# Kernel optimization log

Hardware: AMD Instinct MI355X
Metric: run time of the kernel (lower is better)

Reference implementation:

```python
import jax, jax.numpy as jnp
import numpy as np

N = 50000   # nodes
E = 600000  # edges
D = 128     # in = hidden = out channels
L = 3       # num_layers
LN_EPS = 1e-5


def setup_inputs() -> dict:
    key = jax.random.key(0)
    ks = jax.random.split(key, 4)
    x = jax.random.normal(ks[0], (N, D), dtype=jnp.float32)
    edge_index = jax.random.randint(ks[1], (2, E), 0, N, dtype=jnp.int32)
    # GCNConv linear weights (glorot-ish scale) and biases, one per layer
    Ws = jax.random.normal(ks[2], (L, D, D), dtype=jnp.float32) / np.sqrt(D)
    bs = jnp.zeros((L, D), dtype=jnp.float32)
    # LayerNorm affine params per layer
    ln_w = jnp.ones((L, D), dtype=jnp.float32)
    ln_b = jnp.zeros((L, D), dtype=jnp.float32)
    # PReLU (single shared slope per layer, torch default init 0.25)
    alphas = jnp.full((L,), 0.25, dtype=jnp.float32)
    return {"x": x, "edge_index": edge_index, "Ws": Ws, "bs": bs,
            "ln_w": ln_w, "ln_b": ln_b, "alphas": alphas}


def reference(x, edge_index, Ws, bs, ln_w, ln_b, alphas):
    # --- gcn_norm: add self-loops, symmetric D^{-1/2} (A+I) D^{-1/2} ---
    loop = jnp.arange(N, dtype=edge_index.dtype)
    src = jnp.concatenate([edge_index[0], loop])  # [E+N]
    dst = jnp.concatenate([edge_index[1], loop])  # [E+N]
    deg = jax.ops.segment_sum(jnp.ones_like(dst, dtype=x.dtype), dst,
                              num_segments=N)
    dinv = jnp.where(deg > 0, jax.lax.rsqrt(jnp.maximum(deg, 1.0)), 0.0)
    norm = (dinv[src] * dinv[dst])[:, None]  # [E+N, 1]

    h = x
    for l in range(L):
        # GCNConv: linear -> gather -> scale -> scatter-add -> bias
        h = h @ Ws[l]                                   # [N, D]
        msg = h[src] * norm                             # [E+N, D]
        h = jax.ops.segment_sum(msg, dst, num_segments=N) + bs[l]
        # LayerNorm over feature dim
        mu = jnp.mean(h, axis=-1, keepdims=True)
        var = jnp.mean((h - mu) ** 2, axis=-1, keepdims=True)
        h = (h - mu) * jax.lax.rsqrt(var + LN_EPS) * ln_w[l] + ln_b[l]
        # PReLU
        h = jnp.where(h >= 0, h, alphas[l] * h)
    return h
```

## Files before the change

### kernel.cpp

```cpp
#include <hip/hip_runtime.h>
#include <hip/hip_bf16.h>

#define NN 50000
#define EE 600000
#define DD 128
#define LL 3
#define LN_EPS 1e-5f
#define CAP 64
#define CNTS 16
#define ALD 136
#define POOL 16
#define NTILES (NN / POOL)
#define FILLB ((EE + 255) / 256)

typedef __attribute__((ext_vector_type(8))) short short8;
typedef __attribute__((ext_vector_type(4))) float floatx4;
typedef __attribute__((ext_vector_type(4))) unsigned uintx4;

__device__ inline unsigned short f2bf(float f) {
    union { float f; unsigned u; } a; a.f = f;
    unsigned r = a.u + 0x7fffu + ((a.u >> 16) & 1u);
    return (unsigned short)(r >> 16);
}

__device__ inline uintx4 make_srsrc(const void* p, unsigned bytes) {
    unsigned long long a = (unsigned long long)p;
    uintx4 r;
    r.x = (unsigned)a;
    r.y = (unsigned)(a >> 32);
    r.z = bytes;
    r.w = 0x00020000u;
    return r;
}

__device__ inline uintx4 bload(uintx4 srsrc, unsigned voff) {
    uintx4 r;
    asm volatile("buffer_load_dwordx4 %0, %1, %2, 0 offen"
                 : "=v"(r) : "v"(voff), "s"(srsrc));
    return r;
}

#define WAITV(n) do { \
    asm volatile("s_waitcnt vmcnt(" #n ")" ::: "memory"); \
    __builtin_amdgcn_sched_barrier(0); \
} while (0)


__global__ __launch_bounds__(256) void init_kernel(const float* __restrict__ W,
                                                   unsigned short* __restrict__ Wt,
                                                   int* __restrict__ cnt,
                                                   unsigned short* __restrict__ tbufA,
                                                   unsigned short* __restrict__ tbufB) {
    int tid = blockIdx.x * 256 + threadIdx.x;
    for (int i = tid; i < NN * CNTS / 4; i += gridDim.x * 256)
        ((int4*)cnt)[i] = make_int4(0, 0, 0, 0);
    for (int i = tid; i < 16 * DD / 2; i += gridDim.x * 256) {
        ((int*)&tbufA[(size_t)NN * DD])[i] = 0;
        ((int*)&tbufB[(size_t)NN * DD])[i] = 0;
    }
    for (int i = tid; i < LL * DD * DD; i += gridDim.x * 256) {
        int l = i >> 14, n = (i >> 7) & 127, k = i & 127;
        Wt[i] = f2bf(W[(l << 14) + k * DD + n]);
    }
}


__global__ __launch_bounds__(256) void fill_kernel(
    const int* __restrict__ src, const int* __restrict__ dst,
    int* __restrict__ cnt, int* __restrict__ csrc) {
    int e = blockIdx.x * 256 + threadIdx.x;
    if (e < EE) {
        int d = dst[e];
        int s = src[e];
        int pos = atomicAdd(&cnt[d * CNTS], 1);
        csrc[(size_t)d * CAP + pos] = s;
    }
}


__global__ __launch_bounds__(256) void gemm0_kernel(
    const float* __restrict__ A, const unsigned short* __restrict__ Wt,
    const int* __restrict__ cnt, unsigned short* __restrict__ Cb) {
    __shared__ unsigned short alds[POOL * ALD];
    __shared__ float s_dinv[POOL];
    int tid = threadIdx.x;
    int lane = tid & 63;
    int w = tid >> 6;
    int nodebase = blockIdx.x * POOL;

    if (tid < POOL)
        s_dinv[tid] = rsqrtf((float)(cnt[(nodebase + tid) * CNTS] + 1));

    {
        int row = tid >> 4;
        int kc = (tid & 15) * 8;
        const float* ap = &A[(size_t)(nodebase + row) * DD + kc];
        float4 v0 = *(const float4*)&ap[0];
        float4 v1 = *(const float4*)&ap[4];
        float fv[8] = {v0.x, v0.y, v0.z, v0.w, v1.x, v1.y, v1.z, v1.w};
        unsigned short uv[8];
        #pragma unroll
        for (int q = 0; q < 8; q++) uv[q] = f2bf(fv[q]);
        *(uint4*)&alds[row * ALD + kc] = *(uint4*)&uv[0];
    }
    __syncthreads();

    int cbase = w * 32;
    int kq = (lane >> 4) * 8;
    int mrow = lane & 15;
    floatx4 acc[2] = {{0.f,0.f,0.f,0.f},{0.f,0.f,0.f,0.f}};
    #pragma unroll
    for (int t = 0; t < 4; t++) {
        short8 a = *(const short8*)&alds[mrow * ALD + t * 32 + kq];
        #pragma unroll
        for (int j = 0; j < 2; j++) {
            short8 b = *(const short8*)&Wt[(cbase + j * 16 + (lane & 15)) * DD + t * 32 + kq];
            acc[j] = __builtin_amdgcn_mfma_f32_16x16x32_bf16(a, b, acc[j], 0, 0, 0);
        }
    }
    __syncthreads();

    {
        int r0 = (lane >> 4) * 4;
        #pragma unroll
        for (int i = 0; i < 4; i++) {
            float dvr = s_dinv[r0 + i];
            #pragma unroll
            for (int j = 0; j < 2; j++)
                alds[(r0 + i) * ALD + cbase + j * 16 + (lane & 15)] = f2bf(acc[j][i] * dvr);
        }
    }
    __syncthreads();
    {
        int srow = tid >> 4;
        int scol = (tid & 15) * 8;
        *(uint4*)&Cb[(size_t)(nodebase + srow) * DD + scol] =
            *(uint4*)&alds[srow * ALD + scol];
    }
}


__device__ inline void acc_row(float* acc, uintx4 t) {
    #pragma unroll
    for (int q = 0; q < 4; q++) {
        union { unsigned x; float f; } lo, hi;
        lo.x = t[q] << 16;
        hi.x = t[q] & 0xffff0000u;
        acc[2 * q]     += lo.f;
        acc[2 * q + 1] += hi.f;
    }
}

__device__ inline void agg_node(uintx4 srsrc,
                                const int* __restrict__ cnt, const int* __restrict__ csrc,
                                const float* bv, const float* wv, const float* cv,
                                float alpha, int node, int f8, float* yv, float* dv_out) {
    int deg = cnt[node * CNTS];
    float dv = rsqrtf((float)(deg + 1));
    *dv_out = dv;
    const int* row = &csrc[(size_t)node * CAP];
    unsigned vbase = (unsigned)f8 * 2u;

    int4 i0 = *(const int4*)&row[0];
    int4 i1 = *(const int4*)&row[4];
    int4 i2 = *(const int4*)&row[8];
    int4 i3 = *(const int4*)&row[12];
    int idx[16] = {i0.x, i0.y, i0.z, i0.w, i1.x, i1.y, i1.z, i1.w,
                   i2.x, i2.y, i2.z, i2.w, i3.x, i3.y, i3.z, i3.w};
    unsigned voff[16];
    #pragma unroll
    for (int k = 0; k < 16; k++) {
        int s = (k < deg) ? idx[k] : NN;
        voff[k] = ((unsigned)s << 8) + vbase;
    }
    unsigned voffself = ((unsigned)node << 8) + vbase;

    WAITV(0);
    uintx4 ts = bload(srsrc, voffself);
    uintx4 t0 = bload(srsrc, voff[0]),  t1 = bload(srsrc, voff[1]);
    uintx4 t2 = bload(srsrc, voff[2]),  t3 = bload(srsrc, voff[3]);
    uintx4 t4 = bload(srsrc, voff[4]),  t5 = bload(srsrc, voff[5]);
    uintx4 t6 = bload(srsrc, voff[6]),  t7 = bload(srsrc, voff[7]);

    float acc[8] = {};
    WAITV(8);
    acc_row(acc, ts);
    WAITV(4);
    acc_row(acc, t0); acc_row(acc, t1); acc_row(acc, t2); acc_row(acc, t3);
    uintx4 u0 = bload(srsrc, voff[8]),  u1 = bload(srsrc, voff[9]);
    uintx4 u2 = bload(srsrc, voff[10]), u3 = bload(srsrc, voff[11]);
    WAITV(4);
    acc_row(acc, t4); acc_row(acc, t5); acc_row(acc, t6); acc_row(acc, t7);
    uintx4 w0 = bload(srsrc, voff[12]), w1 = bload(srsrc, voff[13]);
    uintx4 w2 = bload(srsrc, voff[14]), w3 = bload(srsrc, voff[15]);
    WAITV(4);
    acc_row(acc, u0); acc_row(acc, u1); acc_row(acc, u2); acc_row(acc, u3);
    WAITV(0);
    acc_row(acc, w0); acc_row(acc, w1); acc_row(acc, w2); acc_row(acc, w3);

    for (int k = 16; k < deg; k += 4) {
        int4 ss = *(const int4*)&row[k];
        unsigned v0 = ((unsigned)ss.x << 8) + vbase;
        unsigned v1 = ((unsigned)((k + 1 < deg) ? ss.y : NN) << 8) + vbase;
        unsigned v2 = ((unsigned)((k + 2 < deg) ? ss.z : NN) << 8) + vbase;
        unsigned v3 = ((unsigned)((k + 3 < deg) ? ss.w : NN) << 8) + vbase;
        uintx4 a0 = bload(srsrc, v0), a1 = bload(srsrc, v1);
        uintx4 a2 = bload(srsrc, v2), a3 = bload(srsrc, v3);
        WAITV(0);
        acc_row(acc, a0); acc_row(acc, a1); acc_row(acc, a2); acc_row(acc, a3);
    }

    float a[8];
    float s1 = 0.f, s2 = 0.f;
    #pragma unroll
    for (int q = 0; q < 8; q++) {
        a[q] = fmaf(acc[q], dv, bv[q]);
        s1 += a[q]; s2 += a[q] * a[q];
    }
    #pragma unroll
    for (int off = 8; off > 0; off >>= 1) {
        s1 += __shfl_xor(s1, off, 16);
        s2 += __shfl_xor(s2, off, 16);
    }
    float mu = s1 * (1.f / DD);
    float var = s2 * (1.f / DD) - mu * mu;
    float rstd = rsqrtf(var + LN_EPS);
    #pragma unroll
    for (int q = 0; q < 8; q++) {
        float y = (a[q] - mu) * rstd * wv[q] + cv[q];
        yv[q] = (y >= 0.f) ? y : alpha * y;
    }
}


__global__ __launch_bounds__(256) void aggemm_kernel(
    const unsigned short* __restrict__ Tb, const int* __restrict__ cnt,
    const int* __restrict__ csrc,
    const float* __restrict__ bias, const float* __restrict__ lnw,
    const float* __restrict__ lnb, const float* __restrict__ alphas, int layer,
    const unsigned short* __restrict__ Wt, unsigned short* __restrict__ Tout) {
    __shared__ unsigned short alds[POOL * ALD];
    __shared__ float s_dinv[POOL];
    int tid = threadIdx.x;
    int g = tid >> 4;
    int lane16 = tid & 15;
    int f8 = lane16 * 8;
    int nodebase = blockIdx.x * POOL;

    uintx4 srsrc = make_srsrc(Tb, (NN + 1) * DD * 2);

    float4 b0 = *(const float4*)&bias[f8];
    float4 b1 = *(const float4*)&bias[f8 + 4];
    float4 w0 = *(const float4*)&lnw[f8];
    float4 w1 = *(const float4*)&lnw[f8 + 4];
    float4 c0 = *(const float4*)&lnb[f8];
    float4 c1 = *(const float4*)&lnb[f8 + 4];
    float bv[8] = {b0.x, b0.y, b0.z, b0.w, b1.x, b1.y, b1.z, b1.w};
    float wv[8] = {w0.x, w0.y, w0.z, w0.w, w1.x, w1.y, w1.z, w1.w};
    float cv[8] = {c0.x, c0.y, c0.z, c0.w, c1.x, c1.y, c1.z, c1.w};
    float alpha = alphas[layer];

    {
        int node = nodebase + g;
        float yv[8], dv;
        agg_node(srsrc, cnt, csrc, bv, wv, cv, alpha, node, f8, yv, &dv);
        if (lane16 == 0) s_dinv[g] = dv;
        unsigned short pv[8];
        #pragma unroll
        for (int q = 0; q < 8; q++) pv[q] = f2bf(yv[q]);
        *(uint4*)&alds[g * ALD + f8] = *(uint4*)&pv[0];
    }
    __syncthreads();

    int lane = tid & 63;
    int w = tid >> 6;
    int cbase = w * 32;
    int kq = (lane >> 4) * 8;
    int mrow = lane & 15;
    floatx4 acc[2] = {{0.f,0.f,0.f,0.f},{0.f,0.f,0.f,0.f}};
    #pragma unroll
    for (int t = 0; t < 4; t++) {
        short8 a = *(const short8*)&alds[mrow * ALD + t * 32 + kq];
        #pragma unroll
        for (int j = 0; j < 2; j++) {
            short8 b = *(const short8*)&Wt[(cbase + j * 16 + (lane & 15)) * DD + t * 32 + kq];
            acc[j] = __builtin_amdgcn_mfma_f32_16x16x32_bf16(a, b, acc[j], 0, 0, 0);
        }
    }
    __syncthreads();

    {
        int r0 = (lane >> 4) * 4;
        #pragma unroll
        for (int i = 0; i < 4; i++) {
            float dvr = s_dinv[r0 + i];
            #pragma unroll
            for (int j = 0; j < 2; j++)
                alds[(r0 + i) * ALD + cbase + j * 16 + (lane & 15)] = f2bf(acc[j][i] * dvr);
        }
    }
    __syncthreads();
    {
        int srow = tid >> 4;
        int scol = (tid & 15) * 8;
        *(uint4*)&Tout[(size_t)(nodebase + srow) * DD + scol] =
            *(uint4*)&alds[srow * ALD + scol];
    }
}


__global__ __launch_bounds__(256) void agg_final_kernel(
    const unsigned short* __restrict__ Tb, const int* __restrict__ cnt,
    const int* __restrict__ csrc,
    const float* __restrict__ bias, const float* __restrict__ lnw,
    const float* __restrict__ lnb, const float* __restrict__ alphas, int layer,
    float* __restrict__ out) {
    int g = threadIdx.x >> 4;
    int lane16 = threadIdx.x & 15;
    int f8 = lane16 * 8;
    int node = blockIdx.x * POOL + g;

    uintx4 srsrc = make_srsrc(Tb, (NN + 1) * DD * 2);

    float4 b0 = *(const float4*)&bias[f8];
    float4 b1 = *(const float4*)&bias[f8 + 4];
    float4 w0 = *(const float4*)&lnw[f8];
    float4 w1 = *(const float4*)&lnw[f8 + 4];
    float4 c0 = *(const float4*)&lnb[f8];
    float4 c1 = *(const float4*)&lnb[f8 + 4];
    float bv[8] = {b0.x, b0.y, b0.z, b0.w, b1.x, b1.y, b1.z, b1.w};
    float wv[8] = {w0.x, w0.y, w0.z, w0.w, w1.x, w1.y, w1.z, w1.w};
    float cv[8] = {c0.x, c0.y, c0.z, c0.w, c1.x, c1.y, c1.z, c1.w};

    float yv[8], dv;
    agg_node(srsrc, cnt, csrc, bv, wv, cv, alphas[layer], node, f8, yv, &dv);

    float* op = &out[(size_t)node * DD + f8];
    *(float4*)&op[0] = make_float4(yv[0], yv[1], yv[2], yv[3]);
    *(float4*)&op[4] = make_float4(yv[4], yv[5], yv[6], yv[7]);
}


extern "C" void kernel_launch(void* const* d_in, const int* in_sizes, int n_in,
                              void* d_out, int out_size, void* d_ws, size_t ws_size,
                              hipStream_t stream) {
    const float* x    = (const float*)d_in[0];
    const int*   ei   = (const int*)d_in[1];
    const float* Ws   = (const float*)d_in[2];
    const float* bs   = (const float*)d_in[3];
    const float* lnw  = (const float*)d_in[4];
    const float* lnb  = (const float*)d_in[5];
    const float* alphas = (const float*)d_in[6];
    float* out = (float*)d_out;

    const int* src = ei;
    const int* dst = ei + EE;

    char* ws = (char*)d_ws;
    size_t off = 0;
    auto alloc = [&](size_t bytes) -> void* {
        void* p = ws + off;
        off = (off + bytes + 255) & ~(size_t)255;
        return p;
    };
    int* cnt  = (int*)alloc((size_t)NN * CNTS * sizeof(int));
    int* csrc = (int*)alloc((size_t)NN * CAP * sizeof(int));
    unsigned short* wt    = (unsigned short*)alloc((size_t)LL * DD * DD * sizeof(unsigned short));
    unsigned short* tbufA = (unsigned short*)alloc((size_t)(NN + 16) * DD * sizeof(unsigned short));
    unsigned short* tbufB = (unsigned short*)alloc((size_t)(NN + 16) * DD * sizeof(unsigned short));

    init_kernel<<<512, 256, 0, stream>>>(Ws, wt, cnt, tbufA, tbufB);
    fill_kernel<<<FILLB, 256, 0, stream>>>(src, dst, cnt, csrc);
    gemm0_kernel<<<NTILES, 256, 0, stream>>>(x, wt, cnt, tbufA);

    aggemm_kernel<<<NTILES, 256, 0, stream>>>(tbufA, cnt, csrc,
                                              bs + 0 * DD, lnw + 0 * DD, lnb + 0 * DD,
                                              alphas, 0, wt + 1 * DD * DD, tbufB);
    aggemm_kernel<<<NTILES, 256, 0, stream>>>(tbufB, cnt, csrc,
                                              bs + 1 * DD, lnw + 1 * DD, lnb + 1 * DD,
                                              alphas, 1, wt + 2 * DD * DD, tbufA);
    agg_final_kernel<<<NTILES, 256, 0, stream>>>(tbufA, cnt, csrc,
                                                 bs + 2 * DD, lnw + 2 * DD, lnb + 2 * DD,
                                                 alphas, 2, out);
}
```

Measured before the change: 230.0 us.

## Aggregate four nodes per wave with one dword per lane per neighbor

Changes the gather mapping from 16 lanes per node with dwordx4 loads to a full 64-lane wave per node, where each lane loads one dword (two bf16 features). Each wave handles four nodes and issues 68 outstanding loads before staged waits. Neighbor indices are broadcast with readlane, and LayerNorm reduces across the full wave. Degrees above 16 fall back to a slow serial scalar loop. The change is meant to raise memory-level parallelism and coalescing, at the cost of many more load instructions and higher register pressure.

After: 241.3 us. +4.9%, slower.

```diff
diff --git a/kernel.cpp b/kernel.cpp
--- a/kernel.cpp
+++ b/kernel.cpp
@@ -33,17 +33,25 @@
     return r;
 }
 
-__device__ inline uintx4 bload(uintx4 srsrc, unsigned voff) {
-    uintx4 r;
-    asm volatile("buffer_load_dwordx4 %0, %1, %2, 0 offen"
+__device__ inline unsigned bload1(uintx4 srsrc, unsigned voff) {
+    unsigned r;
+    asm volatile("buffer_load_dword %0, %1, %2, 0 offen"
                  : "=v"(r) : "v"(voff), "s"(srsrc));
     return r;
 }
 
-#define WAITV(n) do { \
+#define WAITVM(n) do { \
     asm volatile("s_waitcnt vmcnt(" #n ")" ::: "memory"); \
     __builtin_amdgcn_sched_barrier(0); \
 } while (0)
+
+__device__ inline void upadd(unsigned v, float& x, float& y) {
+    union { unsigned u; float f; } lo, hi;
+    lo.u = v << 16;
+    hi.u = v & 0xffff0000u;
+    x += lo.f;
+    y += hi.f;
+}
 
 
 __global__ __launch_bounds__(256) void init_kernel(const float* __restrict__ W,
@@ -140,96 +148,88 @@
 }
 
 
-__device__ inline void acc_row(float* acc, uintx4 t) {
-    #pragma unroll
-    for (int q = 0; q < 4; q++) {
-        union { unsigned x; float f; } lo, hi;
-        lo.x = t[q] << 16;
-        hi.x = t[q] & 0xffff0000u;
-        acc[2 * q]     += lo.f;
-        acc[2 * q + 1] += hi.f;
-    }
-}
-
-__device__ inline void agg_node(uintx4 srsrc,
-                                const int* __restrict__ cnt, const int* __restrict__ csrc,
-                                const float* bv, const float* wv, const float* cv,
-                                float alpha, int node, int f8, float* yv, float* dv_out) {
-    int deg = cnt[node * CNTS];
-    float dv = rsqrtf((float)(deg + 1));
-    *dv_out = dv;
-    const int* row = &csrc[(size_t)node * CAP];
-    unsigned vbase = (unsigned)f8 * 2u;
-
-    int4 i0 = *(const int4*)&row[0];
-    int4 i1 = *(const int4*)&row[4];
-    int4 i2 = *(const int4*)&row[8];
-    int4 i3 = *(const int4*)&row[12];
-    int idx[16] = {i0.x, i0.y, i0.z, i0.w, i1.x, i1.y, i1.z, i1.w,
-                   i2.x, i2.y, i2.z, i2.w, i3.x, i3.y, i3.z, i3.w};
-    unsigned voff[16];
-    #pragma unroll
-    for (int k = 0; k < 16; k++) {
-        int s = (k < deg) ? idx[k] : NN;
-        voff[k] = ((unsigned)s << 8) + vbase;
-    }
-    unsigned voffself = ((unsigned)node << 8) + vbase;
-
-    WAITV(0);
-    uintx4 ts = bload(srsrc, voffself);
-    uintx4 t0 = bload(srsrc, voff[0]),  t1 = bload(srsrc, voff[1]);
-    uintx4 t2 = bload(srsrc, voff[2]),  t3 = bload(srsrc, voff[3]);
-    uintx4 t4 = bload(srsrc, voff[4]),  t5 = bload(srsrc, voff[5]);
-    uintx4 t6 = bload(srsrc, voff[6]),  t7 = bload(srsrc, voff[7]);
-
-    float acc[8] = {};
-    WAITV(8);
-    acc_row(acc, ts);
-    WAITV(4);
-    acc_row(acc, t0); acc_row(acc, t1); acc_row(acc, t2); acc_row(acc, t3);
-    uintx4 u0 = bload(srsrc, voff[8]),  u1 = bload(srsrc, voff[9]);
-    uintx4 u2 = bload(srsrc, voff[10]), u3 = bload(srsrc, voff[11]);
-    WAITV(4);
-    acc_row(acc, t4); acc_row(acc, t5); acc_row(acc, t6); acc_row(acc, t7);
-    uintx4 w0 = bload(srsrc, voff[12]), w1 = bload(srsrc, voff[13]);
-    uintx4 w2 = bload(srsrc, voff[14]), w3 = bload(srsrc, voff[15]);
-    WAITV(4);
-    acc_row(acc, u0); acc_row(acc, u1); acc_row(acc, u2); acc_row(acc, u3);
-    WAITV(0);
-    acc_row(acc, w0); acc_row(acc, w1); acc_row(acc, w2); acc_row(acc, w3);
-
-    for (int k = 16; k < deg; k += 4) {
-        int4 ss = *(const int4*)&row[k];
-        unsigned v0 = ((unsigned)ss.x << 8) + vbase;
-        unsigned v1 = ((unsigned)((k + 1 < deg) ? ss.y : NN) << 8) + vbase;
-        unsigned v2 = ((unsigned)((k + 2 < deg) ? ss.z : NN) << 8) + vbase;
-        unsigned v3 = ((unsigned)((k + 3 < deg) ? ss.w : NN) << 8) + vbase;
-        uintx4 a0 = bload(srsrc, v0), a1 = bload(srsrc, v1);
-        uintx4 a2 = bload(srsrc, v2), a3 = bload(srsrc, v3);
-        WAITV(0);
-        acc_row(acc, a0); acc_row(acc, a1); acc_row(acc, a2); acc_row(acc, a3);
-    }
-
-    float a[8];
-    float s1 = 0.f, s2 = 0.f;
-    #pragma unroll
-    for (int q = 0; q < 8; q++) {
-        a[q] = fmaf(acc[q], dv, bv[q]);
-        s1 += a[q]; s2 += a[q] * a[q];
-    }
-    #pragma unroll
-    for (int off = 8; off > 0; off >>= 1) {
-        s1 += __shfl_xor(s1, off, 16);
-        s2 += __shfl_xor(s2, off, 16);
+__device__ inline void agg_wave4(uintx4 srsrc, const unsigned short* __restrict__ Tb,
+                                 const int* __restrict__ cnt, const int* __restrict__ csrc,
+                                 int n0, int lane,
+                                 float* A0, float* A1, float* DV) {
+    unsigned l4 = (unsigned)lane << 2;
+    int lane16 = lane & 15;
+
+    int deg[4], iv[4];
+    #pragma unroll
+    for (int j = 0; j < 4; j++)
+        deg[j] = cnt[(size_t)(n0 + j) * CNTS];
+    #pragma unroll
+    for (int j = 0; j < 4; j++) {
+        int raw = csrc[(size_t)(n0 + j) * CAP + lane16];
+        iv[j] = (lane16 < deg[j]) ? raw : NN;
+        DV[j] = rsqrtf((float)(deg[j] + 1));
+    }
+    WAITVM(0);
+
+    unsigned r[4][17];
+    #pragma unroll
+    for (int j = 0; j < 4; j++) {
+        r[j][0] = bload1(srsrc, ((unsigned)(n0 + j) << 8) + l4);
+        #pragma unroll
+        for (int q = 0; q < 16; q++) {
+            int s = __builtin_amdgcn_readlane(iv[j], q);
+            r[j][q + 1] = bload1(srsrc, ((unsigned)s << 8) + l4);
+        }
+    }
+
+    float b0[4], b1[4];
+    WAITVM(51);
+    b0[0] = 0.f; b1[0] = 0.f;
+    #pragma unroll
+    for (int q = 0; q < 17; q++) upadd(r[0][q], b0[0], b1[0]);
+    WAITVM(34);
+    b0[1] = 0.f; b1[1] = 0.f;
+    #pragma unroll
+    for (int q = 0; q < 17; q++) upadd(r[1][q], b0[1], b1[1]);
+    WAITVM(17);
+    b0[2] = 0.f; b1[2] = 0.f;
+    #pragma unroll
+    for (int q = 0; q < 17; q++) upadd(r[2][q], b0[2], b1[2]);
+    WAITVM(0);
+    b0[3] = 0.f; b1[3] = 0.f;
+    #pragma unroll
+    for (int q = 0; q < 17; q++) upadd(r[3][q], b0[3], b1[3]);
+
+    #pragma unroll
+    for (int j = 0; j < 4; j++) {
+        if (deg[j] > 16) {
+            for (int k = 16; k < deg[j]; k++) {
+                int s = csrc[(size_t)(n0 + j) * CAP + k];
+                unsigned v = *(const unsigned*)((const char*)Tb + ((size_t)s << 8) + l4);
+                upadd(v, b0[j], b1[j]);
+            }
+        }
+    }
+    #pragma unroll
+    for (int j = 0; j < 4; j++) { A0[j] = b0[j]; A1[j] = b1[j]; }
+}
+
+__device__ inline void ln_prelu(float acc0, float acc1, float dv,
+                                float bv0, float bv1, float wv0, float wv1,
+                                float cv0, float cv1, float alpha,
+                                float& y0, float& y1) {
+    float a0 = fmaf(acc0, dv, bv0);
+    float a1 = fmaf(acc1, dv, bv1);
+    float s1 = a0 + a1;
+    float s2 = a0 * a0 + a1 * a1;
+    #pragma unroll
+    for (int off = 32; off > 0; off >>= 1) {
+        s1 += __shfl_xor(s1, off, 64);
+        s2 += __shfl_xor(s2, off, 64);
     }
     float mu = s1 * (1.f / DD);
     float var = s2 * (1.f / DD) - mu * mu;
     float rstd = rsqrtf(var + LN_EPS);
-    #pragma unroll
-    for (int q = 0; q < 8; q++) {
-        float y = (a[q] - mu) * rstd * wv[q] + cv[q];
-        yv[q] = (y >= 0.f) ? y : alpha * y;
-    }
+    y0 = (a0 - mu) * rstd * wv0 + cv0;
+    y1 = (a1 - mu) * rstd * wv1 + cv1;
+    y0 = (y0 >= 0.f) ? y0 : alpha * y0;
+    y1 = (y1 >= 0.f) ? y1 : alpha * y1;
 }
 
 
@@ -242,38 +242,34 @@
     __shared__ unsigned short alds[POOL * ALD];
     __shared__ float s_dinv[POOL];
     int tid = threadIdx.x;
-    int g = tid >> 4;
-    int lane16 = tid & 15;
-    int f8 = lane16 * 8;
-    int nodebase = blockIdx.x * POOL;
-
-    uintx4 srsrc = make_srsrc(Tb, (NN + 1) * DD * 2);
-
-    float4 b0 = *(const float4*)&bias[f8];
-    float4 b1 = *(const float4*)&bias[f8 + 4];
-    float4 w0 = *(const float4*)&lnw[f8];
-    float4 w1 = *(const float4*)&lnw[f8 + 4];
-    float4 c0 = *(const float4*)&lnb[f8];
-    float4 c1 = *(const float4*)&lnb[f8 + 4];
-    float bv[8] = {b0.x, b0.y, b0.z, b0.w, b1.x, b1.y, b1.z, b1.w};
-    float wv[8] = {w0.x, w0.y, w0.z, w0.w, w1.x, w1.y, w1.z, w1.w};
-    float cv[8] = {c0.x, c0.y, c0.z, c0.w, c1.x, c1.y, c1.z, c1.w};
-    float alpha = alphas[layer];
-
-    {
-        int node = nodebase + g;
-        float yv[8], dv;
-        agg_node(srsrc, cnt, csrc, bv, wv, cv, alpha, node, f8, yv, &dv);
-        if (lane16 == 0) s_dinv[g] = dv;
-        unsigned short pv[8];
-        #pragma unroll
-        for (int q = 0; q < 8; q++) pv[q] = f2bf(yv[q]);
-        *(uint4*)&alds[g * ALD + f8] = *(uint4*)&pv[0];
-    }
-    __syncthreads();
-
     int lane = tid & 63;
     int w = tid >> 6;
+    int nodebase = blockIdx.x * POOL;
+    int f2 = lane * 2;
+
+    uintx4 srsrc = make_srsrc(Tb, (NN + 1) * DD * 2);
+
+    float2 bp = *(const float2*)&bias[f2];
+    float2 wp = *(const float2*)&lnw[f2];
+    float2 cp = *(const float2*)&lnb[f2];
+    float alpha = alphas[layer];
+
+    {
+        int n0 = nodebase + (w << 2);
+        float A0[4], A1[4], DV[4];
+        agg_wave4(srsrc, Tb, cnt, csrc, n0, lane, A0, A1, DV);
+        #pragma unroll
+        for (int j = 0; j < 4; j++) {
+            float y0, y1;
+            ln_prelu(A0[j], A1[j], DV[j], bp.x, bp.y, wp.x, wp.y, cp.x, cp.y,
+                     alpha, y0, y1);
+            unsigned packed = (unsigned)f2bf(y0) | ((unsigned)f2bf(y1) << 16);
+            *(unsigned*)&alds[((w << 2) + j) * ALD + f2] = packed;
+            if (lane == 0) s_dinv[(w << 2) + j] = DV[j];
+        }
+    }
+    __syncthreads();
+
     int cbase = w * 32;
     int kq = (lane >> 4) * 8;
     int mrow = lane & 15;
@@ -315,29 +311,29 @@
     const float* __restrict__ bias, const float* __restrict__ lnw,
     const float* __restrict__ lnb, const float* __restrict__ alphas, int layer,
     float* __restrict__ out) {
-    int g = threadIdx.x >> 4;
-    int lane16 = threadIdx.x & 15;
-    int f8 = lane16 * 8;
-    int node = blockIdx.x * POOL + g;
+    int tid = threadIdx.x;
+    int lane = tid & 63;
+    int w = tid >> 6;
+    int f2 = lane * 2;
+    int n0 = blockIdx.x * POOL + (w << 2);
 
     uintx4 srsrc = make_srsrc(Tb, (NN + 1) * DD * 2);
 
-    float4 b0 = *(const float4*)&bias[f8];
-    float4 b1 = *(const float4*)&bias[f8 + 4];
-    float4 w0 = *(const float4*)&lnw[f8];
-    float4 w1 = *(const float4*)&lnw[f8 + 4];
-    float4 c0 = *(const float4*)&lnb[f8];
-    float4 c1 = *(const float4*)&lnb[f8 + 4];
-    float bv[8] = {b0.x, b0.y, b0.z, b0.w, b1.x, b1.y, b1.z, b1.w};
-    float wv[8] = {w0.x, w0.y, w0.z, w0.w, w1.x, w1.y, w1.z, w1.w};
-    float cv[8] = {c0.x, c0.y, c0.z, c0.w, c1.x, c1.y, c1.z, c1.w};
-
-    float yv[8], dv;
-    agg_node(srsrc, cnt, csrc, bv, wv, cv, alphas[layer], node, f8, yv, &dv);
-
-    float* op = &out[(size_t)node * DD + f8];
-    *(float4*)&op[0] = make_float4(yv[0], yv[1], yv[2], yv[3]);
-    *(float4*)&op[4] = make_float4(yv[4], yv[5], yv[6], yv[7]);
+    float2 bp = *(const float2*)&bias[f2];
+    float2 wp = *(const float2*)&lnw[f2];
+    float2 cp = *(const float2*)&lnb[f2];
+    float alpha = alphas[layer];
+
+    float A0[4], A1[4], DV[4];
+    agg_wave4(srsrc, Tb, cnt, csrc, n0, lane, A0, A1, DV);
+
+    #pragma unroll
+    for (int j = 0; j < 4; j++) {
+        float y0, y1;
+        ln_prelu(A0[j], A1[j], DV[j], bp.x, bp.y, wp.x, wp.y, cp.x, cp.y,
+                 alpha, y0, y1);
+        *(float2*)&out[(size_t)(n0 + j) * DD + f2] = make_float2(y0, y1);
+    }
 }
 
 
```

## Retile first-layer GEMM to 80 rows per block with 5 waves

Applied to the files above, without the earlier changes.

The first-layer GEMM now processes 80 node rows per block using 320 threads, where each wave owns 16 rows and computes all 128 output columns, instead of 16 rows per block with each wave covering 32 columns. This cuts the block count by a factor of five and amortizes the per-block setup and weight reads across more rows. Each wave now reads the full weight matrix and holds 8 accumulators, which raises register use and per-wave weight traffic.

Measured after the change: 235.3 us. 1.02x slower.

```diff
diff --git a/kernel.cpp b/kernel.cpp
--- a/kernel.cpp
+++ b/kernel.cpp
@@ -11,6 +11,8 @@
 #define ALD 136
 #define POOL 16
 #define NTILES (NN / POOL)
+#define GROWS 80
+#define GBLKS (NN / GROWS)
 #define FILLB ((EE + 255) / 256)
 
 typedef __attribute__((ext_vector_type(8))) short short8;
@@ -78,22 +80,23 @@
 }
 
 
-__global__ __launch_bounds__(256) void gemm0_kernel(
+__global__ __launch_bounds__(320) void gemm0_kernel(
     const float* __restrict__ A, const unsigned short* __restrict__ Wt,
     const int* __restrict__ cnt, unsigned short* __restrict__ Cb) {
-    __shared__ unsigned short alds[POOL * ALD];
-    __shared__ float s_dinv[POOL];
+    __shared__ unsigned short alds[GROWS * ALD];
+    __shared__ float s_dinv[GROWS];
     int tid = threadIdx.x;
     int lane = tid & 63;
     int w = tid >> 6;
-    int nodebase = blockIdx.x * POOL;
-
-    if (tid < POOL)
+    int nodebase = blockIdx.x * GROWS;
+
+    if (tid < GROWS)
         s_dinv[tid] = rsqrtf((float)(cnt[(nodebase + tid) * CNTS] + 1));
 
-    {
-        int row = tid >> 4;
-        int kc = (tid & 15) * 8;
+    #pragma unroll
+    for (int c = tid; c < GROWS * 16; c += 320) {
+        int row = c >> 4;
+        int kc = (c & 15) * 8;
         const float* ap = &A[(size_t)(nodebase + row) * DD + kc];
         float4 v0 = *(const float4*)&ap[0];
         float4 v1 = *(const float4*)&ap[4];
@@ -105,35 +108,36 @@
     }
     __syncthreads();
 
-    int cbase = w * 32;
+    int r0 = w * 16;
     int kq = (lane >> 4) * 8;
-    int mrow = lane & 15;
-    floatx4 acc[2] = {{0.f,0.f,0.f,0.f},{0.f,0.f,0.f,0.f}};
+    int mrow = r0 + (lane & 15);
+    floatx4 acc[8] = {};
     #pragma unroll
     for (int t = 0; t < 4; t++) {
         short8 a = *(const short8*)&alds[mrow * ALD + t * 32 + kq];
         #pragma unroll
-        for (int j = 0; j < 2; j++) {
-            short8 b = *(const short8*)&Wt[(cbase + j * 16 + (lane & 15)) * DD + t * 32 + kq];
+        for (int j = 0; j < 8; j++) {
+            short8 b = *(const short8*)&Wt[(j * 16 + (lane & 15)) * DD + t * 32 + kq];
             acc[j] = __builtin_amdgcn_mfma_f32_16x16x32_bf16(a, b, acc[j], 0, 0, 0);
         }
     }
     __syncthreads();
 
     {
-        int r0 = (lane >> 4) * 4;
+        int rr = r0 + (lane >> 4) * 4;
         #pragma unroll
         for (int i = 0; i < 4; i++) {
-            float dvr = s_dinv[r0 + i];
+            float dvr = s_dinv[rr + i];
             #pragma unroll
-            for (int j = 0; j < 2; j++)
-                alds[(r0 + i) * ALD + cbase + j * 16 + (lane & 15)] = f2bf(acc[j][i] * dvr);
+            for (int j = 0; j < 8; j++)
+                alds[(rr + i) * ALD + j * 16 + (lane & 15)] = f2bf(acc[j][i] * dvr);
         }
     }
     __syncthreads();
-    {
-        int srow = tid >> 4;
-        int scol = (tid & 15) * 8;
+    #pragma unroll
+    for (int c = tid; c < GROWS * 16; c += 320) {
+        int srow = c >> 4;
+        int scol = (c & 15) * 8;
         *(uint4*)&Cb[(size_t)(nodebase + srow) * DD + scol] =
             *(uint4*)&alds[srow * ALD + scol];
     }
@@ -371,7 +375,7 @@
 
     init_kernel<<<512, 256, 0, stream>>>(Ws, wt, cnt, tbufA, tbufB);
     fill_kernel<<<FILLB, 256, 0, stream>>>(src, dst, cnt, csrc);
-    gemm0_kernel<<<NTILES, 256, 0, stream>>>(x, wt, cnt, tbufA);
+    gemm0_kernel<<<GBLKS, 320, 0, stream>>>(x, wt, cnt, tbufA);
 
     aggemm_kernel<<<NTILES, 256, 0, stream>>>(tbufA, cnt, csrc,
                                               bs + 0 * DD, lnw + 0 * DD, lnb + 0 * DD,
```

## Fuse init, edge fill and first GEMM into one cooperative persistent kernel

Applied to the files above, without the earlier changes.

Replaces the three preprocessing launches (zeroing/weight transpose, CSR fill, layer-0 GEMM) with a single cooperative kernel of 2048 blocks that uses grid-wide syncs between phases. The first GEMM's MFMA work is done before the degree counts are final and overlaps with the edge fill, and only the degree scaling waits for the second grid sync. This removes two launch gaps and lets the GEMM overlap with the atomic fill, but cooperative launch limits occupancy to what fits resident and adds grid-barrier costs. If the cooperative launch fails, the old three-kernel path runs instead.

New measurement: 609.7 us. +165.1%, slower.

```diff
diff --git a/kernel.cpp b/kernel.cpp
--- a/kernel.cpp
+++ b/kernel.cpp
@@ -1,5 +1,8 @@
 #include <hip/hip_runtime.h>
 #include <hip/hip_bf16.h>
+#include <hip/hip_cooperative_groups.h>
+
+namespace cg = cooperative_groups;
 
 #define NN 50000
 #define EE 600000
@@ -11,6 +14,7 @@
 #define ALD 136
 #define POOL 16
 #define NTILES (NN / POOL)
+#define PREB 2048
 #define FILLB ((EE + 255) / 256)
 
 typedef __attribute__((ext_vector_type(8))) short short8;
@@ -44,6 +48,124 @@
     asm volatile("s_waitcnt vmcnt(" #n ")" ::: "memory"); \
     __builtin_amdgcn_sched_barrier(0); \
 } while (0)
+
+
+__device__ inline void g0_stage(const float* __restrict__ A, int nodebase,
+                                unsigned short* alds, int tid) {
+    int row = tid >> 4;
+    int kc = (tid & 15) * 8;
+    const float* ap = &A[(size_t)(nodebase + row) * DD + kc];
+    float4 v0 = *(const float4*)&ap[0];
+    float4 v1 = *(const float4*)&ap[4];
+    float fv[8] = {v0.x, v0.y, v0.z, v0.w, v1.x, v1.y, v1.z, v1.w};
+    unsigned short uv[8];
+    #pragma unroll
+    for (int q = 0; q < 8; q++) uv[q] = f2bf(fv[q]);
+    *(uint4*)&alds[row * ALD + kc] = *(uint4*)&uv[0];
+}
+
+__device__ inline void g0_mfma(const unsigned short* alds,
+                               const unsigned short* __restrict__ Wt,
+                               int lane, int w, floatx4* acc) {
+    int cbase = w * 32;
+    int kq = (lane >> 4) * 8;
+    int mrow = lane & 15;
+    #pragma unroll
+    for (int t = 0; t < 4; t++) {
+        short8 a = *(const short8*)&alds[mrow * ALD + t * 32 + kq];
+        #pragma unroll
+        for (int j = 0; j < 2; j++) {
+            short8 b = *(const short8*)&Wt[(cbase + j * 16 + (lane & 15)) * DD + t * 32 + kq];
+            acc[j] = __builtin_amdgcn_mfma_f32_16x16x32_bf16(a, b, acc[j], 0, 0, 0);
+        }
+    }
+}
+
+__device__ inline void g0_transpose(unsigned short* alds, const float* s_dinv,
+                                    int lane, int w, const floatx4* acc) {
+    int cbase = w * 32;
+    int r0 = (lane >> 4) * 4;
+    #pragma unroll
+    for (int i = 0; i < 4; i++) {
+        float dvr = s_dinv[r0 + i];
+        #pragma unroll
+        for (int j = 0; j < 2; j++)
+            alds[(r0 + i) * ALD + cbase + j * 16 + (lane & 15)] = f2bf(acc[j][i] * dvr);
+    }
+}
+
+__device__ inline void g0_store(unsigned short* __restrict__ Cb, int nodebase,
+                                const unsigned short* alds, int tid) {
+    int srow = tid >> 4;
+    int scol = (tid & 15) * 8;
+    *(uint4*)&Cb[(size_t)(nodebase + srow) * DD + scol] =
+        *(uint4*)&alds[srow * ALD + scol];
+}
+
+
+__global__ __launch_bounds__(256, 8) void pre_kernel(
+    const float* __restrict__ A, const float* __restrict__ W,
+    unsigned short* __restrict__ Wt,
+    const int* __restrict__ src, const int* __restrict__ dst,
+    int* __restrict__ cnt, int* __restrict__ csrc,
+    unsigned short* __restrict__ Cb, unsigned short* __restrict__ padB) {
+    cg::grid_group grid = cg::this_grid();
+    __shared__ unsigned short alds[POOL * ALD];
+    __shared__ float s_dinv[POOL];
+    int tid = threadIdx.x;
+    int bid = blockIdx.x;
+    int gid = bid * 256 + tid;
+    const int GS = PREB * 256;
+
+    for (int i = gid; i < NN * CNTS / 4; i += GS)
+        ((int4*)cnt)[i] = make_int4(0, 0, 0, 0);
+    if (gid < 16 * DD / 2) {
+        ((int*)&Cb[(size_t)NN * DD])[gid] = 0;
+        ((int*)&padB[(size_t)NN * DD])[gid] = 0;
+    }
+    for (int i = gid; i < LL * DD * DD; i += GS) {
+        int l = i >> 14, n = (i >> 7) & 127, k = i & 127;
+        Wt[i] = f2bf(W[(l << 14) + k * DD + n]);
+    }
+    int baseA = bid * POOL;
+    g0_stage(A, baseA, alds, tid);
+    grid.sync();
+
+    for (int e = gid; e < EE; e += GS) {
+        int d = dst[e];
+        int s = src[e];
+        int pos = atomicAdd(&cnt[d * CNTS], 1);
+        csrc[(size_t)d * CAP + pos] = s;
+    }
+    int lane = tid & 63;
+    int w = tid >> 6;
+    floatx4 acc[2] = {{0.f,0.f,0.f,0.f},{0.f,0.f,0.f,0.f}};
+    g0_mfma(alds, Wt, lane, w, acc);
+    grid.sync();
+
+    if (tid < POOL)
+        s_dinv[tid] = rsqrtf((float)(cnt[(baseA + tid) * CNTS] + 1));
+    __syncthreads();
+    g0_transpose(alds, s_dinv, lane, w, acc);
+    __syncthreads();
+    g0_store(Cb, baseA, alds, tid);
+
+    int tB = bid + PREB;
+    if (tB < NTILES) {
+        int baseB = tB * POOL;
+        __syncthreads();
+        if (tid < POOL)
+            s_dinv[tid] = rsqrtf((float)(cnt[(baseB + tid) * CNTS] + 1));
+        g0_stage(A, baseB, alds, tid);
+        __syncthreads();
+        floatx4 acc2[2] = {{0.f,0.f,0.f,0.f},{0.f,0.f,0.f,0.f}};
+        g0_mfma(alds, Wt, lane, w, acc2);
+        __syncthreads();
+        g0_transpose(alds, s_dinv, lane, w, acc2);
+        __syncthreads();
+        g0_store(Cb, baseB, alds, tid);
+    }
+}
 
 
 __global__ __launch_bounds__(256) void init_kernel(const float* __restrict__ W,
@@ -64,7 +186,6 @@
     }
 }
 
-
 __global__ __launch_bounds__(256) void fill_kernel(
     const int* __restrict__ src, const int* __restrict__ dst,
     int* __restrict__ cnt, int* __restrict__ csrc) {
@@ -77,7 +198,6 @@
     }
 }
 
-
 __global__ __launch_bounds__(256) void gemm0_kernel(
     const float* __restrict__ A, const unsigned short* __restrict__ Wt,
     const int* __restrict__ cnt, unsigned short* __restrict__ Cb) {
@@ -90,53 +210,14 @@
 
     if (tid < POOL)
         s_dinv[tid] = rsqrtf((float)(cnt[(nodebase + tid) * CNTS] + 1));
-
-    {
-        int row = tid >> 4;
-        int kc = (tid & 15) * 8;
-        const float* ap = &A[(size_t)(nodebase + row) * DD + kc];
-        float4 v0 = *(const float4*)&ap[0];
-        float4 v1 = *(const float4*)&ap[4];
-        float fv[8] = {v0.x, v0.y, v0.z, v0.w, v1.x, v1.y, v1.z, v1.w};
-        unsigned short uv[8];
-        #pragma unroll
-        for (int q = 0; q < 8; q++) uv[q] = f2bf(fv[q]);
-        *(uint4*)&alds[row * ALD + kc] = *(uint4*)&uv[0];
-    }
-    __syncthreads();
-
-    int cbase = w * 32;
-    int kq = (lane >> 4) * 8;
-    int mrow = lane & 15;
+    g0_stage(A, nodebase, alds, tid);
+    __syncthreads();
     floatx4 acc[2] = {{0.f,0.f,0.f,0.f},{0.f,0.f,0.f,0.f}};
-    #pragma unroll
-    for (int t = 0; t < 4; t++) {
-        short8 a = *(const short8*)&alds[mrow * ALD + t * 32 + kq];
-        #pragma unroll
-        for (int j = 0; j < 2; j++) {
-            short8 b = *(const short8*)&Wt[(cbase + j * 16 + (lane & 15)) * DD + t * 32 + kq];
-            acc[j] = __builtin_amdgcn_mfma_f32_16x16x32_bf16(a, b, acc[j], 0, 0, 0);
-        }
-    }
-    __syncthreads();
-
-    {
-        int r0 = (lane >> 4) * 4;
-        #pragma unroll
-        for (int i = 0; i < 4; i++) {
-            float dvr = s_dinv[r0 + i];
-            #pragma unroll
-            for (int j = 0; j < 2; j++)
-                alds[(r0 + i) * ALD + cbase + j * 16 + (lane & 15)] = f2bf(acc[j][i] * dvr);
-        }
-    }
-    __syncthreads();
-    {
-        int srow = tid >> 4;
-        int scol = (tid & 15) * 8;
-        *(uint4*)&Cb[(size_t)(nodebase + srow) * DD + scol] =
-            *(uint4*)&alds[srow * ALD + scol];
-    }
+    g0_mfma(alds, Wt, lane, w, acc);
+    __syncthreads();
+    g0_transpose(alds, s_dinv, lane, w, acc);
+    __syncthreads();
+    g0_store(Cb, nodebase, alds, tid);
 }
 
 
@@ -274,38 +355,13 @@
 
     int lane = tid & 63;
     int w = tid >> 6;
-    int cbase = w * 32;
-    int kq = (lane >> 4) * 8;
-    int mrow = lane & 15;
     floatx4 acc[2] = {{0.f,0.f,0.f,0.f},{0.f,0.f,0.f,0.f}};
-    #pragma unroll
-    for (int t = 0; t < 4; t++) {
-        short8 a = *(const short8*)&alds[mrow * ALD + t * 32 + kq];
-        #pragma unroll
-        for (int j = 0; j < 2; j++) {
-            short8 b = *(const short8*)&Wt[(cbase + j * 16 + (lane & 15)) * DD + t * 32 + kq];
-            acc[j] = __builtin_amdgcn_mfma_f32_16x16x32_bf16(a, b, acc[j], 0, 0, 0);
-        }
-    }
-    __syncthreads();
-
-    {
-        int r0 = (lane >> 4) * 4;
-        #pragma unroll
-        for (int i = 0; i < 4; i++) {
-            float dvr = s_dinv[r0 + i];
-            #pragma unroll
-            for (int j = 0; j < 2; j++)
-                alds[(r0 + i) * ALD + cbase + j * 16 + (lane & 15)] = f2bf(acc[j][i] * dvr);
-        }
-    }
-    __syncthreads();
-    {
-        int srow = tid >> 4;
-        int scol = (tid & 15) * 8;
-        *(uint4*)&Tout[(size_t)(nodebase + srow) * DD + scol] =
-            *(uint4*)&alds[srow * ALD + scol];
-    }
+    g0_mfma(alds, Wt, lane, w, acc);
+    __syncthreads();
+
+    g0_transpose(alds, s_dinv, lane, w, acc);
+    __syncthreads();
+    g0_store(Tout, nodebase, alds, tid);
 }
 
 
@@ -369,9 +425,17 @@
     unsigned short* tbufA = (unsigned short*)alloc((size_t)(NN + 16) * DD * sizeof(unsigned short));
     unsigned short* tbufB = (unsigned short*)alloc((size_t)(NN + 16) * DD * sizeof(unsigned short));
 
-    init_kernel<<<512, 256, 0, stream>>>(Ws, wt, cnt, tbufA, tbufB);
-    fill_kernel<<<FILLB, 256, 0, stream>>>(src, dst, cnt, csrc);
-    gemm0_kernel<<<NTILES, 256, 0, stream>>>(x, wt, cnt, tbufA);
+    {
+        void* ka[] = {(void*)&x, (void*)&Ws, (void*)&wt, (void*)&src, (void*)&dst,
+                      (void*)&cnt, (void*)&csrc, (void*)&tbufA, (void*)&tbufB};
+        hipError_t e = hipLaunchCooperativeKernel((const void*)pre_kernel,
+                                                  dim3(PREB), dim3(256), ka, 0, stream);
+        if (e != hipSuccess) {
+            init_kernel<<<512, 256, 0, stream>>>(Ws, wt, cnt, tbufA, tbufB);
+            fill_kernel<<<FILLB, 256, 0, stream>>>(src, dst, cnt, csrc);
+            gemm0_kernel<<<NTILES, 256, 0, stream>>>(x, wt, cnt, tbufA);
+        }
+    }
 
     aggemm_kernel<<<NTILES, 256, 0, stream>>>(tbufA, cnt, csrc,
                                               bs + 0 * DD, lnw + 0 * DD, lnb + 0 * DD,
```
